# Performance work log

Measured on AMD Instinct MI355X. Metric: run time of the kernel, lower is better.

Reference implementation:

```python
import jax, jax.numpy as jnp
import numpy as np

N_NODES = 100_000
N_EDGES = 1_600_000
HIDDEN = 128
OUT_DIM = 400


def setup_inputs() -> dict:
    key = jax.random.key(0)
    ks = jax.random.split(key, 6)
    x = jax.random.normal(ks[0], (N_NODES, 1), dtype=jnp.float32)
    edge_index = jax.random.randint(ks[1], (2, N_EDGES), 0, N_NODES, dtype=jnp.int32)
    # Glorot-style init for the two GCN weight matrices
    W1 = jax.random.normal(ks[2], (1, HIDDEN), dtype=jnp.float32) * (1.0 / np.sqrt(1 + HIDDEN))
    b1 = jnp.zeros((HIDDEN,), dtype=jnp.float32)
    W2 = jax.random.normal(ks[3], (HIDDEN, OUT_DIM), dtype=jnp.float32) * (1.0 / np.sqrt(HIDDEN + OUT_DIM))
    b2 = jnp.zeros((OUT_DIM,), dtype=jnp.float32)
    return {"x": x, "edge_index": edge_index, "W1": W1, "b1": b1, "W2": W2, "b2": b2}


def _gcn_layer(x, W, b, row, col, norm, num_nodes):
    # PyG GCNConv: out[col] += norm * (x @ W)[row]; then + bias
    h = x @ W                                   # [N, F_out]
    msg = h[row] * norm[:, None]                # [E+N, F_out] gather + scale
    out = jax.ops.segment_sum(msg, col, num_segments=num_nodes)  # scatter-add
    return out + b


def reference(x, edge_index, W1, b1, W2, b2):
    n = x.shape[0]
    loops = jnp.arange(n, dtype=edge_index.dtype)
    row = jnp.concatenate([edge_index[0], loops])  # sources (+ self loops)
    col = jnp.concatenate([edge_index[1], loops])  # destinations (+ self loops)
    # symmetric normalization: deg over destinations, norm = d^-1/2[row] * d^-1/2[col]
    deg = jnp.zeros((n,), dtype=x.dtype).at[col].add(1.0)  # >=1 due to self loops
    dinv = jax.lax.rsqrt(deg)
    norm = dinv[row] * dinv[col]
    h = jax.nn.relu(_gcn_layer(x, W1, b1, row, col, norm, n))
    h = _gcn_layer(h, W2, b2, row, col, norm, n)
    return h.mean(axis=0)  # [OUT_DIM]
```

## Files before the change

kernel.cpp:

```cpp
#include <hip/hip_runtime.h>
#include <math.h>


constexpr int BKT_BITS = 12;
constexpr int BKT_SIZE = 1 << BKT_BITS;
constexpr int NBMAX    = 32;
constexpr int CAP      = 67584;
constexpr int SLICES   = 12;
constexpr int SLICES_D = 24;
constexpr int EPT      = 8;

__global__ void init_cur(int* __restrict__ curC, int* __restrict__ curR,
                         float* __restrict__ total) {
    int t = threadIdx.x;
    if (t < NBMAX) { curC[t] = t * CAP; curR[t] = t * CAP; }
    if (t < 128) total[t] = 0.0f;
}

__global__ void scatter_edges(const int* __restrict__ row, const int* __restrict__ col,
                              int* __restrict__ SC, int* __restrict__ SR,
                              int* __restrict__ curC, int* __restrict__ curR, int E) {
    __shared__ int hC[NBMAX], hR[NBMAX], bC[NBMAX], bR[NBMAX];
    const int TILE = blockDim.x * EPT;
    const int nTiles = (E + TILE - 1) / TILE;
    for (int t = blockIdx.x; t < nTiles; t += gridDim.x) {
        const int myBase = t * TILE + threadIdx.x * EPT;
        int r[EPT], c[EPT];
        if (myBase + EPT <= E) {
            int4 r0 = *reinterpret_cast<const int4*>(row + myBase);
            int4 r1 = *reinterpret_cast<const int4*>(row + myBase + 4);
            int4 c0 = *reinterpret_cast<const int4*>(col + myBase);
            int4 c1 = *reinterpret_cast<const int4*>(col + myBase + 4);
            r[0]=r0.x; r[1]=r0.y; r[2]=r0.z; r[3]=r0.w;
            r[4]=r1.x; r[5]=r1.y; r[6]=r1.z; r[7]=r1.w;
            c[0]=c0.x; c[1]=c0.y; c[2]=c0.z; c[3]=c0.w;
            c[4]=c1.x; c[5]=c1.y; c[6]=c1.z; c[7]=c1.w;
        } else {
#pragma unroll
            for (int j = 0; j < EPT; ++j) {
                int e = myBase + j;
                r[j] = (e < E) ? row[e] : -1;
                c[j] = (e < E) ? col[e] : -1;
            }
        }
        if (threadIdx.x < NBMAX) { hC[threadIdx.x] = 0; hR[threadIdx.x] = 0; }
        __syncthreads();
#pragma unroll
        for (int j = 0; j < EPT; ++j) {
            if (r[j] >= 0) {
                atomicAdd(&hC[c[j] >> BKT_BITS], 1);
                atomicAdd(&hR[r[j] >> BKT_BITS], 1);
            }
        }
        __syncthreads();
        if (threadIdx.x < NBMAX) {
            bC[threadIdx.x] = atomicAdd(&curC[threadIdx.x], hC[threadIdx.x]);
            hC[threadIdx.x] = 0;
            bR[threadIdx.x] = atomicAdd(&curR[threadIdx.x], hR[threadIdx.x]);
            hR[threadIdx.x] = 0;
        }
        __syncthreads();
#pragma unroll
        for (int j = 0; j < EPT; ++j) {
            if (r[j] >= 0) {
                int kb = c[j] >> BKT_BITS;
                int idx = bC[kb] + atomicAdd(&hC[kb], 1);
                if (idx < (kb + 1) * CAP)
                    SC[idx] = ((c[j] & (BKT_SIZE - 1)) << 17) | r[j];
                int kb2 = r[j] >> BKT_BITS;
                int idx2 = bR[kb2] + atomicAdd(&hR[kb2], 1);
                if (idx2 < (kb2 + 1) * CAP)
                    SR[idx2] = ((r[j] & (BKT_SIZE - 1)) << 17) | c[j];
            }
        }
        __syncthreads();
    }
}

__global__ void hist_deg(const int* __restrict__ SC, const int* __restrict__ cur,
                         float* __restrict__ P, int stride) {
    __shared__ float bins[BKT_SIZE];
    const int b = blockIdx.x / SLICES_D, s = blockIdx.x % SLICES_D;
    const int base = b * CAP;
    int len = cur[b] - base;
    len = len < CAP ? len : CAP;
    const int lo = base + (int)((long long)len * s / SLICES_D);
    const int hi = base + (int)((long long)len * (s + 1) / SLICES_D);
    for (int i = threadIdx.x; i < BKT_SIZE; i += blockDim.x) bins[i] = 0.0f;
    __syncthreads();
    for (int e = lo + threadIdx.x; e < hi; e += blockDim.x)
        atomicAdd(&bins[SC[e] >> 17], 1.0f);
    __syncthreads();
    float* dst = P + (size_t)s * stride + b * BKT_SIZE;
    for (int i = threadIdx.x; i < BKT_SIZE; i += blockDim.x) dst[i] = bins[i];
}

__global__ void finalize_deg(const float* __restrict__ Pd, const float* __restrict__ x,
                             float* __restrict__ dinv, float* __restrict__ u,
                             int N, int stride) {
    int i = blockIdx.x * blockDim.x + threadIdx.x;
    if (i >= N) return;
    float d = 1.0f;
    for (int s = 0; s < SLICES_D; ++s) d += Pd[(size_t)s * stride + i];
    float di = rsqrtf(d);
    dinv[i] = di;
    u[i] = di * x[i];
}

__global__ void hist_gather_both(const int* __restrict__ SC, const int* __restrict__ SR,
                                 const int* __restrict__ curC, const int* __restrict__ curR,
                                 const float* __restrict__ u, const float* __restrict__ dinv,
                                 float* __restrict__ Ps, float* __restrict__ Pw,
                                 int stride, int half) {
    __shared__ float bins[BKT_SIZE];
    const bool isW = blockIdx.x >= half;
    const int id = isW ? blockIdx.x - half : blockIdx.x;
    const int* S = isW ? SR : SC;
    const int* cur = isW ? curR : curC;
    const float* val = isW ? dinv : u;
    float* P = isW ? Pw : Ps;
    const int b = id / SLICES, s = id % SLICES;
    const int base = b * CAP;
    int len = cur[b] - base;
    len = len < CAP ? len : CAP;
    const int lo = base + (int)((long long)len * s / SLICES);
    const int hi = base + (int)((long long)len * (s + 1) / SLICES);
    for (int i = threadIdx.x; i < BKT_SIZE; i += blockDim.x) bins[i] = 0.0f;
    __syncthreads();
    for (int e = lo + threadIdx.x; e < hi; e += blockDim.x) {
        int v = S[e];
        atomicAdd(&bins[v >> 17], val[v & 0x1FFFF]);
    }
    __syncthreads();
    float* dst = P + (size_t)s * stride + b * BKT_SIZE;
    for (int i = threadIdx.x; i < BKT_SIZE; i += blockDim.x) dst[i] = bins[i];
}

__global__ void fused_node(const float* __restrict__ Ps, const float* __restrict__ Pw,
                           const float* __restrict__ dinv, const float* __restrict__ x,
                           const float* __restrict__ W1, const float* __restrict__ b1,
                           float* __restrict__ total, int N, int stride) {
    __shared__ float scs[256];
    __shared__ float ws[256];
    __shared__ float red[256];
    const int tid = threadIdx.x;
    const int i = blockIdx.x * 256 + tid;
    float scv = 0.0f, wv = 0.0f;
    if (i < N) {
        float sr = 0.0f, wr = 0.0f;
        for (int s = 0; s < SLICES; ++s) {
            sr += Ps[(size_t)s * stride + i];
            wr += Pw[(size_t)s * stride + i];
        }
        float di = dinv[i];
        scv = di * sr + di * di * x[i];
        wv  = di * (wr + di);
    }
    scs[tid] = scv;
    ws[tid]  = wv;
    __syncthreads();
    const int k = tid & 127;
    const int base = (tid >> 7) * 128;
    const float w1k = W1[k];
    const float b1k = b1[k];
    float acc = 0.0f;
#pragma unroll 4
    for (int j = 0; j < 128; ++j) {
        float h = scs[base + j] * w1k + b1k;
        h = h > 0.0f ? h : 0.0f;
        acc += ws[base + j] * h;
    }
    red[tid] = acc;
    __syncthreads();
    if (tid < 128)
        atomicAdd(&total[k], red[tid] + red[tid + 128]);
}

__global__ void final_out(const float* __restrict__ total,
                          const float* __restrict__ W2, const float* __restrict__ b2,
                          float* __restrict__ out, int OUT, float invN) {
    __shared__ float t[128];
    const int tid = threadIdx.x;
    if (tid < 128) t[tid] = total[tid] * invN;
    __syncthreads();
    const int d = blockIdx.x * 128 + tid;
    if (d < OUT) {
        float acc = b2[d];
#pragma unroll 4
        for (int kk = 0; kk < 128; ++kk) acc += t[kk] * W2[kk * OUT + d];
        out[d] = acc;
    }
}

extern "C" void kernel_launch(void* const* d_in, const int* in_sizes, int n_in,
                              void* d_out, int out_size, void* d_ws, size_t ws_size,
                              hipStream_t stream) {
    const float* x          = (const float*)d_in[0];
    const int*   edge_index = (const int*)  d_in[1];
    const float* W1         = (const float*)d_in[2];
    const float* b1         = (const float*)d_in[3];
    const float* W2         = (const float*)d_in[4];
    const float* b2         = (const float*)d_in[5];
    float* out = (float*)d_out;

    const int N   = in_sizes[0];
    const int E   = in_sizes[1] / 2;
    const int OUT = in_sizes[5];

    const int* row = edge_index;
    const int* col = edge_index + E;

    const int NB = (N + BKT_SIZE - 1) >> BKT_BITS;
    const int stride = NB * BKT_SIZE;

    char* p = (char*)d_ws;
    float* dinv  = (float*)p; p += (size_t)N * 4;
    float* u     = (float*)p; p += (size_t)N * 4;
    float* total = (float*)p; p += 512;
    int*   ints  = (int*)p;   p += 256;
    int*   SC    = (int*)p;   p += (size_t)NB * CAP * 4;
    int*   SR    = (int*)p;   p += (size_t)NB * CAP * 4;
    float* P     = (float*)p;
    float* Ps    = P;
    float* Pw    = P + (size_t)SLICES * stride;

    int* curC = ints;
    int* curR = ints + 32;

    init_cur<<<1, 128, 0, stream>>>(curC, curR, total);
    scatter_edges<<<512, 256, 0, stream>>>(row, col, SC, SR, curC, curR, E);
    hist_deg<<<NB * SLICES_D, 256, 0, stream>>>(SC, curC, P, stride);
    finalize_deg<<<(N + 255) / 256, 256, 0, stream>>>(P, x, dinv, u, N, stride);
    const int half = NB * SLICES;
    hist_gather_both<<<2 * half, 256, 0, stream>>>(SC, SR, curC, curR, u, dinv,
                                                   Ps, Pw, stride, half);
    fused_node<<<(N + 255) / 256, 256, 0, stream>>>(Ps, Pw, dinv, x, W1, b1,
                                                    total, N, stride);
    final_out<<<(OUT + 127) / 128, 128, 0, stream>>>(total, W2, b2, out, OUT,
                                                     1.0f / (float)N);
}
```

Measured before the change: 166.5 us.

## Fuse degree histogram with finalize and fold output GEMV into last block

Degree counting now runs one 1024-thread block per bucket that builds the full histogram in shared memory and writes dinv and u directly. This removes the sliced partial-histogram pass and the separate finalize kernel. The final W2 projection moves into fused_node through a last-block-done atomic counter, which removes another launch. scatter_edges now launches one block per tile instead of 512 persistent blocks. The cost is that the degree pass runs on only NB (about 25) blocks, far fewer than before, and the output GEMV now runs serially in a single block.

New measurement: 257.1 us. +54.4%, slower.

```diff
diff --git a/kernel.cpp b/kernel.cpp
--- a/kernel.cpp
+++ b/kernel.cpp
@@ -7,14 +7,14 @@
 constexpr int NBMAX    = 32;
 constexpr int CAP      = 67584;
 constexpr int SLICES   = 12;
-constexpr int SLICES_D = 24;
 constexpr int EPT      = 8;
 
-__global__ void init_cur(int* __restrict__ curC, int* __restrict__ curR,
-                         float* __restrict__ total) {
+__global__ void init_misc(int* __restrict__ curC, int* __restrict__ curR,
+                          float* __restrict__ total, unsigned* __restrict__ cnt) {
     int t = threadIdx.x;
     if (t < NBMAX) { curC[t] = t * CAP; curR[t] = t * CAP; }
     if (t < 128) total[t] = 0.0f;
+    if (t == 0) *cnt = 0u;
 }
 
 __global__ void scatter_edges(const int* __restrict__ row, const int* __restrict__ col,
@@ -77,34 +77,29 @@
     }
 }
 
-__global__ void hist_deg(const int* __restrict__ SC, const int* __restrict__ cur,
-                         float* __restrict__ P, int stride) {
+__global__ __launch_bounds__(1024)
+void deg_finalize(const int* __restrict__ SC, const int* __restrict__ curC,
+                  const float* __restrict__ x, float* __restrict__ dinv,
+                  float* __restrict__ u, int N) {
     __shared__ float bins[BKT_SIZE];
-    const int b = blockIdx.x / SLICES_D, s = blockIdx.x % SLICES_D;
+    const int b = blockIdx.x;
     const int base = b * CAP;
-    int len = cur[b] - base;
+    int len = curC[b] - base;
     len = len < CAP ? len : CAP;
-    const int lo = base + (int)((long long)len * s / SLICES_D);
-    const int hi = base + (int)((long long)len * (s + 1) / SLICES_D);
-    for (int i = threadIdx.x; i < BKT_SIZE; i += blockDim.x) bins[i] = 0.0f;
-    __syncthreads();
-    for (int e = lo + threadIdx.x; e < hi; e += blockDim.x)
+    for (int i = threadIdx.x; i < BKT_SIZE; i += 1024) bins[i] = 0.0f;
+    __syncthreads();
+    for (int e = base + threadIdx.x; e < base + len; e += 1024)
         atomicAdd(&bins[SC[e] >> 17], 1.0f);
     __syncthreads();
-    float* dst = P + (size_t)s * stride + b * BKT_SIZE;
-    for (int i = threadIdx.x; i < BKT_SIZE; i += blockDim.x) dst[i] = bins[i];
-}
-
-__global__ void finalize_deg(const float* __restrict__ Pd, const float* __restrict__ x,
-                             float* __restrict__ dinv, float* __restrict__ u,
-                             int N, int stride) {
-    int i = blockIdx.x * blockDim.x + threadIdx.x;
-    if (i >= N) return;
-    float d = 1.0f;
-    for (int s = 0; s < SLICES_D; ++s) d += Pd[(size_t)s * stride + i];
-    float di = rsqrtf(d);
-    dinv[i] = di;
-    u[i] = di * x[i];
+    const int nb = b << BKT_BITS;
+    for (int i = threadIdx.x; i < BKT_SIZE; i += 1024) {
+        int node = nb + i;
+        if (node < N) {
+            float di = rsqrtf(1.0f + bins[i]);
+            dinv[node] = di;
+            u[node] = di * x[node];
+        }
+    }
 }
 
 __global__ void hist_gather_both(const int* __restrict__ SC, const int* __restrict__ SR,
@@ -139,10 +134,14 @@
 __global__ void fused_node(const float* __restrict__ Ps, const float* __restrict__ Pw,
                            const float* __restrict__ dinv, const float* __restrict__ x,
                            const float* __restrict__ W1, const float* __restrict__ b1,
-                           float* __restrict__ total, int N, int stride) {
+                           float* __restrict__ total, int N, int stride,
+                           const float* __restrict__ W2, const float* __restrict__ b2,
+                           float* __restrict__ out, int OUT, float invN,
+                           unsigned* __restrict__ cnt) {
     __shared__ float scs[256];
     __shared__ float ws[256];
     __shared__ float red[256];
+    __shared__ unsigned lastFlag;
     const int tid = threadIdx.x;
     const int i = blockIdx.x * 256 + tid;
     float scv = 0.0f, wv = 0.0f;
@@ -174,21 +173,22 @@
     __syncthreads();
     if (tid < 128)
         atomicAdd(&total[k], red[tid] + red[tid + 128]);
-}
-
-__global__ void final_out(const float* __restrict__ total,
-                          const float* __restrict__ W2, const float* __restrict__ b2,
-                          float* __restrict__ out, int OUT, float invN) {
-    __shared__ float t[128];
-    const int tid = threadIdx.x;
-    if (tid < 128) t[tid] = total[tid] * invN;
-    __syncthreads();
-    const int d = blockIdx.x * 128 + tid;
-    if (d < OUT) {
-        float acc = b2[d];
+    __threadfence();
+    __syncthreads();
+    if (tid == 0)
+        lastFlag = (atomicAdd(cnt, 1u) == (unsigned)(gridDim.x - 1)) ? 1u : 0u;
+    __syncthreads();
+    if (lastFlag) {
+        __shared__ float tv[128];
+        if (tid < 128)
+            tv[tid] = atomicAdd(&total[tid], 0.0f) * invN;
+        __syncthreads();
+        for (int d = tid; d < OUT; d += 256) {
+            float a = b2[d];
 #pragma unroll 4
-        for (int kk = 0; kk < 128; ++kk) acc += t[kk] * W2[kk * OUT + d];
-        out[d] = acc;
+            for (int kk = 0; kk < 128; ++kk) a += tv[kk] * W2[kk * OUT + d];
+            out[d] = a;
+        }
     }
 }
 
@@ -217,7 +217,7 @@
     float* dinv  = (float*)p; p += (size_t)N * 4;
     float* u     = (float*)p; p += (size_t)N * 4;
     float* total = (float*)p; p += 512;
-    int*   ints  = (int*)p;   p += 256;
+    int*   ints  = (int*)p;   p += 512;
     int*   SC    = (int*)p;   p += (size_t)NB * CAP * 4;
     int*   SR    = (int*)p;   p += (size_t)NB * CAP * 4;
     float* P     = (float*)p;
@@ -226,16 +226,19 @@
 
     int* curC = ints;
     int* curR = ints + 32;
-
-    init_cur<<<1, 128, 0, stream>>>(curC, curR, total);
-    scatter_edges<<<512, 256, 0, stream>>>(row, col, SC, SR, curC, curR, E);
-    hist_deg<<<NB * SLICES_D, 256, 0, stream>>>(SC, curC, P, stride);
-    finalize_deg<<<(N + 255) / 256, 256, 0, stream>>>(P, x, dinv, u, N, stride);
+    unsigned* cnt = (unsigned*)(ints + 64);
+
+    const int TILE   = 256 * EPT;
+    const int nTiles = (E + TILE - 1) / TILE;
+
+    init_misc<<<1, 128, 0, stream>>>(curC, curR, total, cnt);
+    scatter_edges<<<nTiles, 256, 0, stream>>>(row, col, SC, SR, curC, curR, E);
+    deg_finalize<<<NB, 1024, 0, stream>>>(SC, curC, x, dinv, u, N);
     const int half = NB * SLICES;
     hist_gather_both<<<2 * half, 256, 0, stream>>>(SC, SR, curC, curR, u, dinv,
                                                    Ps, Pw, stride, half);
     fused_node<<<(N + 255) / 256, 256, 0, stream>>>(Ps, Pw, dinv, x, W1, b1,
-                                                    total, N, stride);
-    final_out<<<(OUT + 127) / 128, 128, 0, stream>>>(total, W2, b2, out, OUT,
-                                                     1.0f / (float)N);
-}
+                                                    total, N, stride,
+                                                    W2, b2, out, OUT,
+                                                    1.0f / (float)N, cnt);
+}
```
